# Kernel optimization log

Measured on AMD Instinct MI355X. Metric: run time of the kernel, lower is better.

## Reference

```python
import jax, jax.numpy as jnp
import numpy as np

EPS = 1e-6


def setup_inputs() -> dict:
    key = jax.random.key(0)
    k1, k2 = jax.random.split(key)
    B, K, N, d = 4, 16, 2048, 256
    return {
        "img_f": jax.random.normal(k1, (B, K, d), dtype=jnp.float32),
        "text_f": jax.random.normal(k2, (N, K, d), dtype=jnp.float32),
        "r": jnp.zeros((4,), dtype=jnp.float32),
        "alp": jnp.array([0.5], dtype=jnp.float32),
        "scale": jnp.array([1.0], dtype=jnp.float32),
        "logits_scales": jnp.array([0.5], dtype=jnp.float32),
    }


def _rc_dist_ItoT(I, T, alpha, beta):
    # I: (B,K,d) images, T: (N,K,d) texts -> dist (B,N)
    B, K, d = I.shape
    lam = (B / d) * jnp.exp(alpha) + EPS
    rho = jnp.exp(beta)
    ItI = jnp.einsum('bkd,bke->bde', I, I)                      # (B,d,d)
    Minv = jnp.linalg.inv(ItI + lam * jnp.eye(d, dtype=I.dtype))
    A = jnp.einsum('bde,bke->bdk', Minv, I)                      # (B,d,K) = Minv @ I^T
    # T_bar[b,n] = I[b] @ A[b] @ T[n]; fuse P = I @ A (B,K,K) to avoid (B,N,d,d) W.
    P = jnp.einsum('bkd,bdj->bkj', I, A)                         # (B,K,K)
    T_bar = jnp.einsum('bkj,njd->bnkd', P, T) * rho              # (B,N,K,d)
    diff = T_bar - T[None]
    return -jnp.sum(diff * diff, axis=-1).mean(axis=-1)          # (B,N)


def _rc_dist_TtoI(I, T, alpha, beta):
    # per-text ridge projector applied to images -> dist (B,N)
    N, K, d = T.shape
    lam = (N / d) * jnp.exp(alpha) + EPS
    rho = jnp.exp(beta)
    TtT = jnp.einsum('nkd,nke->nde', T, T)                       # (N,d,d)
    Minv = jnp.linalg.inv(TtT + lam * jnp.eye(d, dtype=T.dtype))
    A = jnp.einsum('nde,nke->ndk', Minv, T)                      # (N,d,K)
    Q = jnp.einsum('nkd,ndj->nkj', T, A)                         # (N,K,K)
    I_bar = jnp.einsum('nkj,bjd->nbkd', Q, I) * rho              # (N,B,K,d)
    diff = I_bar - I[None]
    return (-jnp.sum(diff * diff, axis=-1).mean(axis=-1)).T      # (B,N)


def reference(img_f, text_f, r, alp, scale, logits_scales):
    d1 = _rc_dist_ItoT(img_f, text_f, r[0], r[1])
    d2 = _rc_dist_TtoI(img_f, text_f, r[2], r[3])
    rc_dist = alp * d1 + (1.0 - alp) * d2
    logits = rc_dist * scale
    logits_pre = jax.nn.log_softmax(logits, axis=1)
    return logits_pre, jax.nn.sigmoid(logits_scales)
```

## Files before the change

### kernel.cpp

```cpp
#include <hip/hip_runtime.h>
#include <math.h>

#define Bq 4
#define Kq 16
#define Nq 2048
#define Dq 256

typedef float f32x4 __attribute__((ext_vector_type(4)));
typedef short s16x8 __attribute__((ext_vector_type(8)));
typedef unsigned int u32;

union frag_u { s16x8 v; u32 w[4]; };

static __device__ __forceinline__ u32 cvtpk(float a, float b) {
    u32 r;
    asm("v_cvt_pk_bf16_f32 %0, %1, %2" : "=v"(r) : "v"(a), "v"(b));
    return r;
}

static __device__ __forceinline__ void cvt2(float a, float b, u32* hw, u32* lw) {
    const u32 h = cvtpk(a, b);
    const float h0 = __uint_as_float(h << 16);
    const float h1 = __uint_as_float(h & 0xFFFF0000u);
    *hw = h;
    *lw = cvtpk(a - h0, b - h1);
}

static __device__ __forceinline__ void conv8(const float4 a, const float4 b,
                                             s16x8* hi, s16x8* lo) {
    frag_u H, L;
    cvt2(a.x, a.y, &H.w[0], &L.w[0]);
    cvt2(a.z, a.w, &H.w[1], &L.w[1]);
    cvt2(b.x, b.y, &H.w[2], &L.w[2]);
    cvt2(b.z, b.w, &H.w[3], &L.w[3]);
    *hi = H.v; *lo = L.v;
}

static __device__ __forceinline__ float rdlane(float x, int l) {
    return __uint_as_float((u32)__builtin_amdgcn_readlane((int)__float_as_uint(x), l));
}

#define MFMA(A, B, C) __builtin_amdgcn_mfma_f32_16x16x32_bf16((A), (B), (C), 0, 0, 0)

__global__ __launch_bounds__(256, 2) void fused_kernel(const float* __restrict__ img,
                                                       const float* __restrict__ text,
                                                       const float* __restrict__ r,
                                                       const float* __restrict__ alp,
                                                       const float* __restrict__ scale,
                                                       float* __restrict__ logits) {
    __shared__ __align__(16) float scratch[4][2][16][20];
    __shared__ __align__(16) f32x4 shS1[4][64];
    __shared__ __align__(16) f32x4 shGI[4][64];

    const int tid  = threadIdx.x;
    const int w    = tid >> 6, lane = tid & 63;
    const int arow = lane & 15, kgrp = lane >> 4, ccol = arow;
    const int n    = blockIdx.x * 4 + w;
    const bool isT = (lane & 16) != 0;
    const int  sys = isT ? 1 : 0;

    const float* baseI = img  + w * (Kq * Dq) + arow * Dq + kgrp * 8;
    const float* baseT = text + n * (Kq * Dq) + arow * Dq + kgrp * 8;
    float4 xi[16], xt[16];
#pragma unroll
    for (int c = 0; c < 8; ++c) {
        xi[2 * c]     = *reinterpret_cast<const float4*>(baseI + c * 32);
        xi[2 * c + 1] = *reinterpret_cast<const float4*>(baseI + c * 32 + 4);
    }
#pragma unroll
    for (int c = 0; c < 8; ++c) {
        xt[2 * c]     = *reinterpret_cast<const float4*>(baseT + c * 32);
        xt[2 * c + 1] = *reinterpret_cast<const float4*>(baseT + c * 32 + 4);
    }
    __builtin_amdgcn_sched_barrier(0);

    const float lamI = (float(Bq) / float(Dq)) * expf(r[0]) + 1e-6f;
    const float rhoI = expf(r[1]);
    const float lamT = (float(Nq) / float(Dq)) * expf(r[2]) + 1e-6f;
    const float rhoT = expf(r[3]);

    f32x4 gI = {0.f, 0.f, 0.f, 0.f};
#pragma unroll
    for (int c = 0; c < 8; ++c) {
        s16x8 hi, lo;
        conv8(xi[2 * c], xi[2 * c + 1], &hi, &lo);
        gI = MFMA(hi, hi, gI); gI = MFMA(hi, lo, gI); gI = MFMA(lo, hi, gI);
    }
    f32x4 gT = {0.f, 0.f, 0.f, 0.f};
#pragma unroll
    for (int c = 0; c < 8; ++c) {
        s16x8 hi, lo;
        conv8(xt[2 * c], xt[2 * c + 1], &hi, &lo);
        gT = MFMA(hi, hi, gT); gT = MFMA(hi, lo, gT); gT = MFMA(lo, hi, gT);
    }

    float (*Gc)[16][20] = scratch[w];
    *reinterpret_cast<f32x4*>(&Gc[0][ccol][kgrp * 4]) = gI;
    *reinterpret_cast<f32x4*>(&Gc[1][ccol][kgrp * 4]) = gT;
    __builtin_amdgcn_wave_barrier();

    const int j = arow;
    float A[16], rhs[16];
    {
        const float lam = isT ? lamT : lamI;
        const float rho = isT ? rhoT : rhoI;
        const float* col = &Gc[sys][j][0];
        const f32x4 c0 = *reinterpret_cast<const f32x4*>(col + 0);
        const f32x4 c1 = *reinterpret_cast<const f32x4*>(col + 4);
        const f32x4 c2 = *reinterpret_cast<const f32x4*>(col + 8);
        const f32x4 c3 = *reinterpret_cast<const f32x4*>(col + 12);
        float g[16];
#pragma unroll
        for (int q = 0; q < 4; ++q) {
            g[q] = c0[q]; g[4 + q] = c1[q]; g[8 + q] = c2[q]; g[12 + q] = c3[q];
        }
#pragma unroll
        for (int i = 0; i < 16; ++i) {
            const float dv = (i == j) ? lam : 0.f;
            A[i]   = g[i] + dv;
            rhs[i] = (rho - 1.f) * g[i] - dv;
        }
    }
    __builtin_amdgcn_wave_barrier();

#pragma unroll
    for (int k = 0; k < Kq; ++k) {
        const float pI = rdlane(A[k], k);
        const float pT = rdlane(A[k], 16 + k);
        const float pinv = 1.0f / (isT ? pT : pI);
        A[k]   *= pinv;
        rhs[k] *= pinv;
#pragma unroll
        for (int i = 0; i < 16; ++i) {
            if (i == k) continue;
            const float uI = rdlane(A[i], k);
            const float uT = rdlane(A[i], 16 + k);
            const float fac = isT ? uT : uI;
            A[i]   = fmaf(-fac, A[k],   A[i]);
            rhs[i] = fmaf(-fac, rhs[k], rhs[i]);
        }
    }

    float (*Mr)[16][20] = scratch[w];
#pragma unroll
    for (int i = 0; i < 16; ++i) Mr[sys][i][j] = rhs[i];
    __builtin_amdgcn_wave_barrier();

    frag_u HImg, LImg, HTxt, LTxt;
#pragma unroll
    for (int e = 0; e < 8; e += 2) {
        const int kk = (kgrp & 1) * 8 + e;
        const bool vld = (lane < 32);
        const float i0 = vld ? Mr[0][arow][kk]     : 0.f;
        const float i1 = vld ? Mr[0][arow][kk + 1] : 0.f;
        const float t0 = vld ? Mr[1][arow][kk]     : 0.f;
        const float t1 = vld ? Mr[1][arow][kk + 1] : 0.f;
        cvt2(i0, i1, &HImg.w[e >> 1], &LImg.w[e >> 1]);
        cvt2(t0, t1, &HTxt.w[e >> 1], &LTxt.w[e >> 1]);
    }
    f32x4 sI = {0.f, 0.f, 0.f, 0.f}, sT = {0.f, 0.f, 0.f, 0.f};
    sI = MFMA(HImg.v, HImg.v, sI); sI = MFMA(HImg.v, LImg.v, sI); sI = MFMA(LImg.v, HImg.v, sI);
    sT = MFMA(HTxt.v, HTxt.v, sT); sT = MFMA(HTxt.v, LTxt.v, sT); sT = MFMA(LTxt.v, HTxt.v, sT);

    shS1[w][lane] = sI;
    shGI[w][lane] = gI;
    __syncthreads();

    float p[8];
#pragma unroll
    for (int b = 0; b < 4; ++b) {
        const f32x4 s1 = shS1[b][lane];
        const f32x4 gi = shGI[b][lane];
        p[b]     = s1.x * gT.x + s1.y * gT.y + s1.z * gT.z + s1.w * gT.w;
        p[4 + b] = gi.x * sT.x + gi.y * sT.y + gi.z * sT.z + gi.w * sT.w;
    }
#pragma unroll
    for (int off = 32; off; off >>= 1) {
#pragma unroll
        for (int q = 0; q < 8; ++q) p[q] += __shfl_down(p[q], off, 64);
    }
    if (lane == 0) {
        const float a = alp[0], sc = scale[0];
#pragma unroll
        for (int b = 0; b < 4; ++b) {
            const float d1 = -p[b] * (1.f / Kq);
            const float d2 = -p[4 + b] * (1.f / Kq);
            logits[b * Nq + n] = sc * (a * d1 + (1.f - a) * d2);
        }
    }
}

__global__ __launch_bounds__(256) void softmax_kernel(const float* __restrict__ logits,
                                                      const float* __restrict__ lsc,
                                                      float* __restrict__ out) {
    const int b   = blockIdx.x;
    const int tid = threadIdx.x;
    const float* row = logits + b * Nq;
    __shared__ float sh[4];
    float v[8];
    float mx = -INFINITY;
#pragma unroll
    for (int q = 0; q < 8; ++q) {
        v[q] = row[tid + q * 256];
        mx = fmaxf(mx, v[q]);
    }
#pragma unroll
    for (int off = 32; off; off >>= 1) mx = fmaxf(mx, __shfl_down(mx, off, 64));
    if ((tid & 63) == 0) sh[tid >> 6] = mx;
    __syncthreads();
    mx = fmaxf(fmaxf(sh[0], sh[1]), fmaxf(sh[2], sh[3]));

    float sum = 0.f;
#pragma unroll
    for (int q = 0; q < 8; ++q) sum += expf(v[q] - mx);
#pragma unroll
    for (int off = 32; off; off >>= 1) sum += __shfl_down(sum, off, 64);
    __syncthreads();
    if ((tid & 63) == 0) sh[tid >> 6] = sum;
    __syncthreads();
    sum = sh[0] + sh[1] + sh[2] + sh[3];

    const float lse = mx + logf(sum);
#pragma unroll
    for (int q = 0; q < 8; ++q) out[b * Nq + tid + q * 256] = v[q] - lse;
    if (b == 0 && tid == 0) out[Bq * Nq] = 1.f / (1.f + expf(-lsc[0]));
}

extern "C" void kernel_launch(void* const* d_in, const int* in_sizes, int n_in,
                              void* d_out, int out_size, void* d_ws, size_t ws_size,
                              hipStream_t stream) {
    const float* img   = (const float*)d_in[0];
    const float* text  = (const float*)d_in[1];
    const float* r     = (const float*)d_in[2];
    const float* alp   = (const float*)d_in[3];
    const float* scale = (const float*)d_in[4];
    const float* lsc   = (const float*)d_in[5];
    float* ws  = (float*)d_ws;
    float* out = (float*)d_out;

    fused_kernel<<<Nq / 4, 256, 0, stream>>>(img, text, r, alp, scale, ws);
    softmax_kernel<<<Bq, 256, 0, stream>>>(ws, lsc, out);
}
```

Before: 22.93 us.

## Split image solve into its own kernel and fuse softmax via last-block atomic

The image-side Gram and ridge solve move into a small 4-block kernel, so each text block no longer recomputes all four image systems with lanes split between image and text. The text kernel reads the precomputed image results from workspace, solves only its own text system with simpler readlane pivots, and the last block, picked with an atomic counter, runs the log-softmax inline in place of a separate softmax launch. This trades redundant per-block image work and one kernel launch for an extra small serial launch and a single-block softmax tail behind a threadfence/atomic.

```diff
diff --git a/kernel.cpp b/kernel.cpp
--- a/kernel.cpp
+++ b/kernel.cpp
@@ -11,6 +11,7 @@
 typedef unsigned int u32;
 
 union frag_u { s16x8 v; u32 w[4]; };
+
 
 static __device__ __forceinline__ u32 cvtpk(float a, float b) {
     u32 r;
@@ -40,145 +41,159 @@
     return __uint_as_float((u32)__builtin_amdgcn_readlane((int)__float_as_uint(x), l));
 }
 
+static __device__ __forceinline__ float4 gload4(const float* __restrict__ p) {
+    float4 v;
+    asm volatile("global_load_dwordx4 %0, %1, off" : "=v"(v) : "v"(p) : "memory");
+    return v;
+}
+
 #define MFMA(A, B, C) __builtin_amdgcn_mfma_f32_16x16x32_bf16((A), (B), (C), 0, 0, 0)
 
-__global__ __launch_bounds__(256, 2) void fused_kernel(const float* __restrict__ img,
-                                                       const float* __restrict__ text,
-                                                       const float* __restrict__ r,
-                                                       const float* __restrict__ alp,
-                                                       const float* __restrict__ scale,
-                                                       float* __restrict__ logits) {
-    __shared__ __align__(16) float scratch[4][2][16][20];
-    __shared__ __align__(16) f32x4 shS1[4][64];
-    __shared__ __align__(16) f32x4 shGI[4][64];
-
-    const int tid  = threadIdx.x;
-    const int w    = tid >> 6, lane = tid & 63;
-    const int arow = lane & 15, kgrp = lane >> 4, ccol = arow;
-    const int n    = blockIdx.x * 4 + w;
-    const bool isT = (lane & 16) != 0;
-    const int  sys = isT ? 1 : 0;
-
-    const float* baseI = img  + w * (Kq * Dq) + arow * Dq + kgrp * 8;
-    const float* baseT = text + n * (Kq * Dq) + arow * Dq + kgrp * 8;
-    float4 xi[16], xt[16];
-#pragma unroll
-    for (int c = 0; c < 8; ++c) {
-        xi[2 * c]     = *reinterpret_cast<const float4*>(baseI + c * 32);
-        xi[2 * c + 1] = *reinterpret_cast<const float4*>(baseI + c * 32 + 4);
-    }
-#pragma unroll
-    for (int c = 0; c < 8; ++c) {
-        xt[2 * c]     = *reinterpret_cast<const float4*>(baseT + c * 32);
-        xt[2 * c + 1] = *reinterpret_cast<const float4*>(baseT + c * 32 + 4);
-    }
-    __builtin_amdgcn_sched_barrier(0);
-
-    const float lamI = (float(Bq) / float(Dq)) * expf(r[0]) + 1e-6f;
-    const float rhoI = expf(r[1]);
-    const float lamT = (float(Nq) / float(Dq)) * expf(r[2]) + 1e-6f;
-    const float rhoT = expf(r[3]);
-
-    f32x4 gI = {0.f, 0.f, 0.f, 0.f};
+static __device__ __forceinline__ f32x4 gram(const float4* x) {
+    f32x4 g = {0.f, 0.f, 0.f, 0.f};
 #pragma unroll
     for (int c = 0; c < 8; ++c) {
         s16x8 hi, lo;
-        conv8(xi[2 * c], xi[2 * c + 1], &hi, &lo);
-        gI = MFMA(hi, hi, gI); gI = MFMA(hi, lo, gI); gI = MFMA(lo, hi, gI);
-    }
-    f32x4 gT = {0.f, 0.f, 0.f, 0.f};
-#pragma unroll
-    for (int c = 0; c < 8; ++c) {
-        s16x8 hi, lo;
-        conv8(xt[2 * c], xt[2 * c + 1], &hi, &lo);
-        gT = MFMA(hi, hi, gT); gT = MFMA(hi, lo, gT); gT = MFMA(lo, hi, gT);
-    }
-
-    float (*Gc)[16][20] = scratch[w];
-    *reinterpret_cast<f32x4*>(&Gc[0][ccol][kgrp * 4]) = gI;
-    *reinterpret_cast<f32x4*>(&Gc[1][ccol][kgrp * 4]) = gT;
+        conv8(x[2 * c], x[2 * c + 1], &hi, &lo);
+        g = MFMA(hi, hi, g); g = MFMA(hi, lo, g); g = MFMA(lo, hi, g);
+    }
+    return g;
+}
+
+static __device__ __forceinline__ f32x4 solve_S(f32x4 g, float lam, float rho,
+                                                float (*scr)[20], int lane) {
+    const int ccol = lane & 15, kgrp = lane >> 4, arow = ccol, j = ccol;
+    *reinterpret_cast<f32x4*>(&scr[ccol][kgrp * 4]) = g;
     __builtin_amdgcn_wave_barrier();
-
-    const int j = arow;
     float A[16], rhs[16];
     {
-        const float lam = isT ? lamT : lamI;
-        const float rho = isT ? rhoT : rhoI;
-        const float* col = &Gc[sys][j][0];
+        const float* col = &scr[j][0];
         const f32x4 c0 = *reinterpret_cast<const f32x4*>(col + 0);
         const f32x4 c1 = *reinterpret_cast<const f32x4*>(col + 4);
         const f32x4 c2 = *reinterpret_cast<const f32x4*>(col + 8);
         const f32x4 c3 = *reinterpret_cast<const f32x4*>(col + 12);
-        float g[16];
+        float gv[16];
 #pragma unroll
         for (int q = 0; q < 4; ++q) {
-            g[q] = c0[q]; g[4 + q] = c1[q]; g[8 + q] = c2[q]; g[12 + q] = c3[q];
+            gv[q] = c0[q]; gv[4 + q] = c1[q]; gv[8 + q] = c2[q]; gv[12 + q] = c3[q];
         }
 #pragma unroll
         for (int i = 0; i < 16; ++i) {
             const float dv = (i == j) ? lam : 0.f;
-            A[i]   = g[i] + dv;
-            rhs[i] = (rho - 1.f) * g[i] - dv;
+            A[i]   = gv[i] + dv;
+            rhs[i] = (rho - 1.f) * gv[i] - dv;
         }
     }
     __builtin_amdgcn_wave_barrier();
 
 #pragma unroll
     for (int k = 0; k < Kq; ++k) {
-        const float pI = rdlane(A[k], k);
-        const float pT = rdlane(A[k], 16 + k);
-        const float pinv = 1.0f / (isT ? pT : pI);
+        const float pinv = 1.0f / rdlane(A[k], k);
         A[k]   *= pinv;
         rhs[k] *= pinv;
 #pragma unroll
         for (int i = 0; i < 16; ++i) {
             if (i == k) continue;
-            const float uI = rdlane(A[i], k);
-            const float uT = rdlane(A[i], 16 + k);
-            const float fac = isT ? uT : uI;
+            const float fac = rdlane(A[i], k);
             A[i]   = fmaf(-fac, A[k],   A[i]);
             rhs[i] = fmaf(-fac, rhs[k], rhs[i]);
         }
     }
-
-    float (*Mr)[16][20] = scratch[w];
-#pragma unroll
-    for (int i = 0; i < 16; ++i) Mr[sys][i][j] = rhs[i];
+#pragma unroll
+    for (int i = 0; i < 16; ++i) scr[i][j] = rhs[i];
     __builtin_amdgcn_wave_barrier();
 
-    frag_u HImg, LImg, HTxt, LTxt;
+    frag_u H, L;
 #pragma unroll
     for (int e = 0; e < 8; e += 2) {
         const int kk = (kgrp & 1) * 8 + e;
         const bool vld = (lane < 32);
-        const float i0 = vld ? Mr[0][arow][kk]     : 0.f;
-        const float i1 = vld ? Mr[0][arow][kk + 1] : 0.f;
-        const float t0 = vld ? Mr[1][arow][kk]     : 0.f;
-        const float t1 = vld ? Mr[1][arow][kk + 1] : 0.f;
-        cvt2(i0, i1, &HImg.w[e >> 1], &LImg.w[e >> 1]);
-        cvt2(t0, t1, &HTxt.w[e >> 1], &LTxt.w[e >> 1]);
-    }
-    f32x4 sI = {0.f, 0.f, 0.f, 0.f}, sT = {0.f, 0.f, 0.f, 0.f};
-    sI = MFMA(HImg.v, HImg.v, sI); sI = MFMA(HImg.v, LImg.v, sI); sI = MFMA(LImg.v, HImg.v, sI);
-    sT = MFMA(HTxt.v, HTxt.v, sT); sT = MFMA(HTxt.v, LTxt.v, sT); sT = MFMA(LTxt.v, HTxt.v, sT);
-
-    shS1[w][lane] = sI;
-    shGI[w][lane] = gI;
-    __syncthreads();
+        const float m0 = vld ? scr[arow][kk]     : 0.f;
+        const float m1 = vld ? scr[arow][kk + 1] : 0.f;
+        cvt2(m0, m1, &H.w[e >> 1], &L.w[e >> 1]);
+    }
+    f32x4 s = {0.f, 0.f, 0.f, 0.f};
+    s = MFMA(H.v, H.v, s); s = MFMA(H.v, L.v, s); s = MFMA(L.v, H.v, s);
+    return s;
+}
+
+__global__ __launch_bounds__(64) void img_kernel(const float* __restrict__ img,
+                                                 const float* __restrict__ r,
+                                                 float* __restrict__ ws) {
+    __shared__ __align__(16) float scr[16][20];
+    const int lane = threadIdx.x;
+    const int b    = blockIdx.x;
+    const int arow = lane & 15, kgrp = lane >> 4;
+    if (b == 0 && lane == 0) *reinterpret_cast<int*>(ws + 10240) = 0;
+
+    const float* base = img + b * (Kq * Dq) + arow * Dq + kgrp * 8;
+    float4 x[16];
+#pragma unroll
+    for (int c = 0; c < 8; ++c) {
+        x[2 * c]     = gload4(base + c * 32);
+        x[2 * c + 1] = gload4(base + c * 32 + 4);
+    }
+    asm volatile("s_waitcnt vmcnt(0)" ::: "memory");
+    __builtin_amdgcn_sched_barrier(0);
+
+    const float lam = (float(Bq) / float(Dq)) * expf(r[0]) + 1e-6f;
+    const float rho = expf(r[1]);
+    const f32x4 g = gram(x);
+    const f32x4 s = solve_S(g, lam, rho, scr, lane);
+    reinterpret_cast<f32x4*>(ws)[b * 64 + lane]        = s;
+    reinterpret_cast<f32x4*>(ws + 1024)[b * 64 + lane] = g;
+}
+
+__global__ __launch_bounds__(256, 2) void text_kernel(const float* __restrict__ text,
+                                                      const float* __restrict__ r,
+                                                      const float* __restrict__ alp,
+                                                      const float* __restrict__ scale,
+                                                      const float* __restrict__ lsc,
+                                                      float* __restrict__ ws,
+                                                      float* __restrict__ out) {
+    __shared__ __align__(16) float scr[4][16][20];
+    __shared__ int lastFlag;
+    const int tid  = threadIdx.x;
+    const int w    = tid >> 6, lane = tid & 63;
+    const int arow = lane & 15, kgrp = lane >> 4;
+    const int n    = blockIdx.x * 4 + w;
+
+    const float* baseT = text + n * (Kq * Dq) + arow * Dq + kgrp * 8;
+    float4 xt[16];
+#pragma unroll
+    for (int c = 0; c < 8; ++c) {
+        xt[2 * c]     = gload4(baseT + c * 32);
+        xt[2 * c + 1] = gload4(baseT + c * 32 + 4);
+    }
+    float4 s1v[4], giv[4];
+#pragma unroll
+    for (int b = 0; b < 4; ++b) {
+        s1v[b] = gload4(ws + (b * 64 + lane) * 4);
+        giv[b] = gload4(ws + 1024 + (b * 64 + lane) * 4);
+    }
+    asm volatile("s_waitcnt vmcnt(8)" ::: "memory");
+    __builtin_amdgcn_sched_barrier(0);
+
+    const float lamT = (float(Nq) / float(Dq)) * expf(r[2]) + 1e-6f;
+    const float rhoT = expf(r[3]);
+    const f32x4 gT = gram(xt);
+    const f32x4 sT = solve_S(gT, lamT, rhoT, scr[w], lane);
+
+    asm volatile("s_waitcnt vmcnt(0)" ::: "memory");
+    __builtin_amdgcn_sched_barrier(0);
 
     float p[8];
 #pragma unroll
     for (int b = 0; b < 4; ++b) {
-        const f32x4 s1 = shS1[b][lane];
-        const f32x4 gi = shGI[b][lane];
-        p[b]     = s1.x * gT.x + s1.y * gT.y + s1.z * gT.z + s1.w * gT.w;
-        p[4 + b] = gi.x * sT.x + gi.y * sT.y + gi.z * sT.z + gi.w * sT.w;
+        p[b]     = s1v[b].x * gT[0] + s1v[b].y * gT[1] + s1v[b].z * gT[2] + s1v[b].w * gT[3];
+        p[4 + b] = giv[b].x * sT[0] + giv[b].y * sT[1] + giv[b].z * sT[2] + giv[b].w * sT[3];
     }
 #pragma unroll
     for (int off = 32; off; off >>= 1) {
 #pragma unroll
         for (int q = 0; q < 8; ++q) p[q] += __shfl_down(p[q], off, 64);
     }
+    float* logits = ws + 2048;
     if (lane == 0) {
         const float a = alp[0], sc = scale[0];
 #pragma unroll
@@ -188,42 +203,34 @@
             logits[b * Nq + n] = sc * (a * d1 + (1.f - a) * d2);
         }
     }
-}
-
-__global__ __launch_bounds__(256) void softmax_kernel(const float* __restrict__ logits,
-                                                      const float* __restrict__ lsc,
-                                                      float* __restrict__ out) {
-    const int b   = blockIdx.x;
-    const int tid = threadIdx.x;
-    const float* row = logits + b * Nq;
-    __shared__ float sh[4];
-    float v[8];
+
+    __threadfence();
+    __syncthreads();
+    if (tid == 0)
+        lastFlag = (atomicAdd(reinterpret_cast<int*>(ws + 10240), 1) == (Nq / 4 - 1));
+    __syncthreads();
+    if (!lastFlag) return;
+    __threadfence();
+
+    const float* row = logits + w * Nq;
+    float v[32];
     float mx = -INFINITY;
 #pragma unroll
-    for (int q = 0; q < 8; ++q) {
-        v[q] = row[tid + q * 256];
+    for (int q = 0; q < 32; ++q) {
+        v[q] = row[lane + q * 64];
         mx = fmaxf(mx, v[q]);
     }
 #pragma unroll
-    for (int off = 32; off; off >>= 1) mx = fmaxf(mx, __shfl_down(mx, off, 64));
-    if ((tid & 63) == 0) sh[tid >> 6] = mx;
-    __syncthreads();
-    mx = fmaxf(fmaxf(sh[0], sh[1]), fmaxf(sh[2], sh[3]));
-
+    for (int off = 32; off; off >>= 1) mx = fmaxf(mx, __shfl_xor(mx, off, 64));
     float sum = 0.f;
 #pragma unroll
-    for (int q = 0; q < 8; ++q) sum += expf(v[q] - mx);
-#pragma unroll
-    for (int off = 32; off; off >>= 1) sum += __shfl_down(sum, off, 64);
-    __syncthreads();
-    if ((tid & 63) == 0) sh[tid >> 6] = sum;
-    __syncthreads();
-    sum = sh[0] + sh[1] + sh[2] + sh[3];
-
+    for (int q = 0; q < 32; ++q) sum += expf(v[q] - mx);
+#pragma unroll
+    for (int off = 32; off; off >>= 1) sum += __shfl_xor(sum, off, 64);
     const float lse = mx + logf(sum);
 #pragma unroll
-    for (int q = 0; q < 8; ++q) out[b * Nq + tid + q * 256] = v[q] - lse;
-    if (b == 0 && tid == 0) out[Bq * Nq] = 1.f / (1.f + expf(-lsc[0]));
+    for (int q = 0; q < 32; ++q) out[w * Nq + lane + q * 64] = v[q] - lse;
+    if (tid == 0) out[Bq * Nq] = 1.f / (1.f + expf(-lsc[0]));
 }
 
 extern "C" void kernel_launch(void* const* d_in, const int* in_sizes, int n_in,
@@ -238,6 +245,6 @@
     float* ws  = (float*)d_ws;
     float* out = (float*)d_out;
 
-    fused_kernel<<<Nq / 4, 256, 0, stream>>>(img, text, r, alp, scale, ws);
-    softmax_kernel<<<Bq, 256, 0, stream>>>(ws, lsc, out);
-}
+    img_kernel<<<Bq, 64, 0, stream>>>(img, r, ws);
+    text_kernel<<<Nq / 4, 256, 0, stream>>>(text, r, alp, scale, lsc, ws, out);
+}
```

After: 55.80 us. +143.4%, slower.
